# Kernel tuning notes

Measured on AMD Instinct MI355X. Metric: run time of the kernel, lower is better.

The kernel has to match this reference:

```python
import jax, jax.numpy as jnp
import numpy as np

EPS = 1e-7  # K.epsilon()
B, S, W1, W2, D = 256, 4, 64, 128, 300
HID = 4


def setup_inputs() -> dict:
    key = jax.random.key(0)
    k1, k2, k3, k4, k5, k6, k7 = jax.random.split(key, 7)
    return {
        "tuple1": jax.random.normal(k1, (B, S, W1, D), dtype=jnp.float32),
        "tuple2": jax.random.normal(k2, (B, S, W2, D), dtype=jnp.float32),
        "mask1": jax.random.randint(k3, (B, S, W1), 0, 2, dtype=jnp.int32),
        "mask2": jax.random.randint(k4, (B, S, W2), 0, 2, dtype=jnp.int32),
        "threshold": jax.random.normal(k5, (), dtype=jnp.float32),
        "W_hidden": jax.random.normal(k6, (S, HID), dtype=jnp.float32) * 0.5,
        "W_score": jax.random.normal(k7, (HID, 1), dtype=jnp.float32) * 0.5,
    }


def reference(tuple1, tuple2, mask1, mask2, threshold, W_hidden, W_score):
    # Pairwise dot-product similarity between every tuple1 word and tuple2 word per slot.
    sim = jnp.einsum("bswd,bsvd->bswv", tuple1, tuple2)  # (B, S, W1, W2)
    m1 = mask1.astype(jnp.float32)
    m2 = mask2.astype(jnp.float32)
    overlap = (sim >= threshold).astype(jnp.float32)
    overlap = overlap * m1[:, :, :, None] * m2[:, :, None, :]
    slot_overlap = jnp.sum(overlap, axis=(2, 3))  # (B, S)
    count1 = jnp.sum(m1, axis=2)  # (B, S)
    divisor = jnp.where(count1 == 0, EPS, count1)
    normalized = slot_overlap / divisor  # (B, S)
    h = jnp.tanh(normalized @ W_hidden)  # (B, HID)
    return jax.nn.sigmoid(h @ W_score)  # (B, 1)
```

## Files before the change

kernel.cpp:

```cpp
#include <hip/hip_runtime.h>
#include <math.h>

#define B_   256
#define S_   4
#define W1_  64
#define W2_  128
#define D_   300
#define HID_ 4

typedef float          fx4   __attribute__((ext_vector_type(4)));
typedef short          s16x8 __attribute__((ext_vector_type(8)));
typedef unsigned int   ux4   __attribute__((ext_vector_type(4)));

__device__ __forceinline__ unsigned bf16_rne(float x) {
    unsigned u = __float_as_uint(x);
    return (u + 0x7FFFu + ((u >> 16) & 1u)) >> 16;
}

__device__ __forceinline__ void cvt8(const fx4 x0, const fx4 x1, s16x8& hi, s16x8& lo) {
    ux4 hu, lu;
#pragma unroll
    for (int p = 0; p < 4; ++p) {
        float a = (p < 2) ? x0[2 * p]     : x1[2 * p - 4];
        float b = (p < 2) ? x0[2 * p + 1] : x1[2 * p - 3];
        unsigned ha = bf16_rne(a), hb = bf16_rne(b);
        float haf = __uint_as_float(ha << 16);
        float hbf = __uint_as_float(hb << 16);
        unsigned la = bf16_rne(a - haf), lb = bf16_rne(b - hbf);
        hu[p] = ha | (hb << 16);
        lu[p] = la | (lb << 16);
    }
    hi = __builtin_bit_cast(s16x8, hu);
    lo = __builtin_bit_cast(s16x8, lu);
}

template <int OFF>
__device__ __forceinline__ void gload(fx4& d, const float* p) {
    asm volatile("global_load_dwordx4 %0, %1, off offset:%c2"
                 : "=v"(d) : "v"(p), "i"(OFF));
}

#define FENCE  __builtin_amdgcn_sched_barrier(0)
#define WAIT24 do { asm volatile("s_waitcnt vmcnt(24)" ::: "memory"); FENCE; } while (0)
#define WAIT12 do { asm volatile("s_waitcnt vmcnt(12)" ::: "memory"); FENCE; } while (0)
#define WAIT0  do { asm volatile("s_waitcnt vmcnt(0)"  ::: "memory"); FENCE; } while (0)

#define ISSUE(T, AA, BB) do { \
    gload<(T)*128>(AA[0][0], aP0); gload<(T)*128+16>(AA[0][1], aP0); \
    gload<(T)*128>(AA[1][0], aP1); gload<(T)*128+16>(AA[1][1], aP1); \
    gload<(T)*128>(BB[0][0], bP0); gload<(T)*128+16>(BB[0][1], bP0); \
    gload<(T)*128>(BB[1][0], bP1); gload<(T)*128+16>(BB[1][1], bP1); \
    gload<(T)*128>(BB[2][0], bP2); gload<(T)*128+16>(BB[2][1], bP2); \
    gload<(T)*128>(BB[3][0], bP3); gload<(T)*128+16>(BB[3][1], bP3); \
    FENCE; } while (0)

__global__ __launch_bounds__(256, 2) void sim_count_mfma(
    const float* __restrict__ t1, const float* __restrict__ t2,
    const int* __restrict__ m1, const int* __restrict__ m2,
    const float* __restrict__ thr_p, int* __restrict__ cnt)
{
    const int slot = blockIdx.x;
    const int tid  = threadIdx.x;
    const int l    = tid & 63;
    const int w    = tid >> 6;
    const int rowHalf = w >> 1, colHalf = w & 1;
    const int lr   = l & 15;
    const int lg8  = (l >> 4) * 8;

    const float* t1b = t1 + (size_t)slot * W1_ * D_;
    const float* t2b = t2 + (size_t)slot * W2_ * D_;
    const float* aP0 = t1b + (size_t)(rowHalf * 32 +  0 + lr) * D_ + lg8;
    const float* aP1 = t1b + (size_t)(rowHalf * 32 + 16 + lr) * D_ + lg8;
    const float* bP0 = t2b + (size_t)(colHalf * 64 +  0 + lr) * D_ + lg8;
    const float* bP1 = t2b + (size_t)(colHalf * 64 + 16 + lr) * D_ + lg8;
    const float* bP2 = t2b + (size_t)(colHalf * 64 + 32 + lr) * D_ + lg8;
    const float* bP3 = t2b + (size_t)(colHalf * 64 + 48 + lr) * D_ + lg8;

    fx4 acc[2][4];
#pragma unroll
    for (int rt = 0; rt < 2; ++rt)
#pragma unroll
        for (int ct = 0; ct < 4; ++ct) {
            fx4 z; z[0] = 0.f; z[1] = 0.f; z[2] = 0.f; z[3] = 0.f;
            acc[rt][ct] = z;
        }

    auto compute = [&](fx4 (&SA)[2][2], fx4 (&SB)[4][2]) {
        s16x8 ah[2], al[2];
#pragma unroll
        for (int rt = 0; rt < 2; ++rt) cvt8(SA[rt][0], SA[rt][1], ah[rt], al[rt]);
#pragma unroll
        for (int ct = 0; ct < 4; ++ct) {
            s16x8 bh, bl;
            cvt8(SB[ct][0], SB[ct][1], bh, bl);
#pragma unroll
            for (int rt = 0; rt < 2; ++rt) {
                acc[rt][ct] = __builtin_amdgcn_mfma_f32_16x16x32_bf16(ah[rt], bh, acc[rt][ct], 0, 0, 0);
                acc[rt][ct] = __builtin_amdgcn_mfma_f32_16x16x32_bf16(ah[rt], bl, acc[rt][ct], 0, 0, 0);
                acc[rt][ct] = __builtin_amdgcn_mfma_f32_16x16x32_bf16(al[rt], bh, acc[rt][ct], 0, 0, 0);
            }
        }
    };

    fx4 A0[2][2], B0[4][2], A1[2][2], B1[4][2], A2[2][2], B2[4][2];

    ISSUE(0, A0, B0);
    ISSUE(1, A1, B1);
    ISSUE(2, A2, B2);
    WAIT24; compute(A0, B0); FENCE; ISSUE(3, A0, B0);
    WAIT24; compute(A1, B1); FENCE; ISSUE(4, A1, B1);
    WAIT24; compute(A2, B2); FENCE; ISSUE(5, A2, B2);
    WAIT24; compute(A0, B0); FENCE; ISSUE(6, A0, B0);
    WAIT24; compute(A1, B1); FENCE; ISSUE(7, A1, B1);
    WAIT24; compute(A2, B2); FENCE; ISSUE(8, A2, B2);
    WAIT24; compute(A0, B0); FENCE;
    WAIT12; compute(A1, B1); FENCE;
    WAIT0;  compute(A2, B2); FENCE;

    {
        fx4 z; z[0] = 0.f; z[1] = 0.f; z[2] = 0.f; z[3] = 0.f;
        A0[0][0] = z; A0[0][1] = z; A0[1][0] = z; A0[1][1] = z;
        B0[0][0] = z; B0[0][1] = z; B0[1][0] = z; B0[1][1] = z;
        B0[2][0] = z; B0[2][1] = z; B0[3][0] = z; B0[3][1] = z;
        if (lg8 < 16) {
            A0[0][0] = *(const fx4*)(aP0 + 288);
            A0[1][0] = *(const fx4*)(aP1 + 288);
            B0[0][0] = *(const fx4*)(bP0 + 288);
            B0[1][0] = *(const fx4*)(bP1 + 288);
            B0[2][0] = *(const fx4*)(bP2 + 288);
            B0[3][0] = *(const fx4*)(bP3 + 288);
        }
        if (lg8 == 0) {
            A0[0][1] = *(const fx4*)(aP0 + 292);
            A0[1][1] = *(const fx4*)(aP1 + 292);
            B0[0][1] = *(const fx4*)(bP0 + 292);
            B0[1][1] = *(const fx4*)(bP1 + 292);
            B0[2][1] = *(const fx4*)(bP2 + 292);
            B0[3][1] = *(const fx4*)(bP3 + 292);
        }
        compute(A0, B0);
    }

    const float thr = *thr_p;
    int am[2][4];
#pragma unroll
    for (int rt = 0; rt < 2; ++rt)
#pragma unroll
        for (int r = 0; r < 4; ++r)
            am[rt][r] = m1[slot * W1_ + rowHalf * 32 + rt * 16 + (l >> 4) * 4 + r];
    int bm[4];
#pragma unroll
    for (int ct = 0; ct < 4; ++ct)
        bm[ct] = m2[slot * W2_ + colHalf * 64 + ct * 16 + lr];

    int lc = 0;
#pragma unroll
    for (int rt = 0; rt < 2; ++rt)
#pragma unroll
        for (int ct = 0; ct < 4; ++ct)
#pragma unroll
            for (int r = 0; r < 4; ++r)
                lc += ((acc[rt][ct][r] >= thr) & (am[rt][r] != 0) & (bm[ct] != 0)) ? 1 : 0;
#pragma unroll
    for (int o = 32; o > 0; o >>= 1) lc += __shfl_down(lc, o);
    if (l == 0) atomicAdd(&cnt[slot], lc);
}

__global__ __launch_bounds__(256) void finalize_head(
    const int* __restrict__ cnt, const int* __restrict__ m1,
    const float* __restrict__ Wh,
    const float* __restrict__ Ws,
    float* __restrict__ out)
{
    int b = blockIdx.x * blockDim.x + threadIdx.x;
    if (b >= B_) return;
    float n[4];
#pragma unroll
    for (int s = 0; s < 4; ++s) {
        const int slot = b * 4 + s;
        int nA = 0;
        const int4* mp = (const int4*)(m1 + slot * W1_);
#pragma unroll
        for (int g = 0; g < 16; ++g) {
            int4 v = mp[g];
            nA += (v.x != 0) + (v.y != 0) + (v.z != 0) + (v.w != 0);
        }
        const float divisor = (nA == 0) ? 1e-7f : (float)nA;
        n[s] = (float)cnt[slot] / divisor;
    }
    float score = 0.f;
#pragma unroll
    for (int j = 0; j < HID_; ++j) {
        float h = n[0] * Wh[0 * HID_ + j] + n[1] * Wh[1 * HID_ + j]
                + n[2] * Wh[2 * HID_ + j] + n[3] * Wh[3 * HID_ + j];
        h = tanhf(h);
        score += h * Ws[j];
    }
    out[b] = 1.f / (1.f + expf(-score));
}

extern "C" void kernel_launch(void* const* d_in, const int* in_sizes, int n_in,
                              void* d_out, int out_size, void* d_ws, size_t ws_size,
                              hipStream_t stream)
{
    const float* t1  = (const float*)d_in[0];
    const float* t2  = (const float*)d_in[1];
    const int*   m1  = (const int*)d_in[2];
    const int*   m2  = (const int*)d_in[3];
    const float* thr = (const float*)d_in[4];
    const float* Wh  = (const float*)d_in[5];
    const float* Ws  = (const float*)d_in[6];
    float* out = (float*)d_out;
    int*   cnt = (int*)d_ws;

    hipMemsetAsync(cnt, 0, B_ * S_ * sizeof(int), stream);
    sim_count_mfma<<<B_ * S_, 256, 0, stream>>>(t1, t2, m1, m2, thr, cnt);
    finalize_head<<<1, 256, 0, stream>>>(cnt, m1, Wh, Ws, out);
}
```

Before: 306.9 us.

## Split each slot across eight blocks with one MFMA tile per wave

Each slot's 64x128 similarity matrix is now split over 8 blocks, and each wave computes a single 16x16 tile with a 4-deep load pipeline. Occupancy is raised to 4 blocks per CU. The goal is more parallelism and latency hiding on a latency-bound kernel. The tail K-chunk is folded into the prefetch pipeline using in-bounds loads and lane masking. The trade-off is more redundant global/L2 loads of A and B rows and more atomics.

```diff
diff --git a/kernel.cpp b/kernel.cpp
--- a/kernel.cpp
+++ b/kernel.cpp
@@ -41,129 +41,90 @@
 }
 
 #define FENCE  __builtin_amdgcn_sched_barrier(0)
-#define WAIT24 do { asm volatile("s_waitcnt vmcnt(24)" ::: "memory"); FENCE; } while (0)
-#define WAIT12 do { asm volatile("s_waitcnt vmcnt(12)" ::: "memory"); FENCE; } while (0)
-#define WAIT0  do { asm volatile("s_waitcnt vmcnt(0)"  ::: "memory"); FENCE; } while (0)
+#define WAITN(N) do { asm volatile("s_waitcnt vmcnt(" #N ")" ::: "memory"); FENCE; } while (0)
 
-#define ISSUE(T, AA, BB) do { \
-    gload<(T)*128>(AA[0][0], aP0); gload<(T)*128+16>(AA[0][1], aP0); \
-    gload<(T)*128>(AA[1][0], aP1); gload<(T)*128+16>(AA[1][1], aP1); \
-    gload<(T)*128>(BB[0][0], bP0); gload<(T)*128+16>(BB[0][1], bP0); \
-    gload<(T)*128>(BB[1][0], bP1); gload<(T)*128+16>(BB[1][1], bP1); \
-    gload<(T)*128>(BB[2][0], bP2); gload<(T)*128+16>(BB[2][1], bP2); \
-    gload<(T)*128>(BB[3][0], bP3); gload<(T)*128+16>(BB[3][1], bP3); \
-    FENCE; } while (0)
-
-__global__ __launch_bounds__(256, 2) void sim_count_mfma(
+__global__ __launch_bounds__(256, 4) void sim_count_mfma(
     const float* __restrict__ t1, const float* __restrict__ t2,
     const int* __restrict__ m1, const int* __restrict__ m2,
     const float* __restrict__ thr_p, int* __restrict__ cnt)
 {
-    const int slot = blockIdx.x;
+    const int slot = blockIdx.x >> 3;
+    const int p8   = blockIdx.x & 7;
     const int tid  = threadIdx.x;
     const int l    = tid & 63;
     const int w    = tid >> 6;
-    const int rowHalf = w >> 1, colHalf = w & 1;
+    const int rt   = (p8 >> 2) * 2 + (w >> 1);
+    const int ct   = (p8 & 3) * 2 + (w & 1);
     const int lr   = l & 15;
     const int lg8  = (l >> 4) * 8;
 
-    const float* t1b = t1 + (size_t)slot * W1_ * D_;
-    const float* t2b = t2 + (size_t)slot * W2_ * D_;
-    const float* aP0 = t1b + (size_t)(rowHalf * 32 +  0 + lr) * D_ + lg8;
-    const float* aP1 = t1b + (size_t)(rowHalf * 32 + 16 + lr) * D_ + lg8;
-    const float* bP0 = t2b + (size_t)(colHalf * 64 +  0 + lr) * D_ + lg8;
-    const float* bP1 = t2b + (size_t)(colHalf * 64 + 16 + lr) * D_ + lg8;
-    const float* bP2 = t2b + (size_t)(colHalf * 64 + 32 + lr) * D_ + lg8;
-    const float* bP3 = t2b + (size_t)(colHalf * 64 + 48 + lr) * D_ + lg8;
+    const float* aP = t1 + (size_t)slot * W1_ * D_ + (size_t)(rt * 16 + lr) * D_ + lg8;
+    const float* bP = t2 + (size_t)slot * W2_ * D_ + (size_t)(ct * 16 + lr) * D_ + lg8;
 
-    fx4 acc[2][4];
-#pragma unroll
-    for (int rt = 0; rt < 2; ++rt)
-#pragma unroll
-        for (int ct = 0; ct < 4; ++ct) {
-            fx4 z; z[0] = 0.f; z[1] = 0.f; z[2] = 0.f; z[3] = 0.f;
-            acc[rt][ct] = z;
-        }
+    fx4 acc; acc[0] = 0.f; acc[1] = 0.f; acc[2] = 0.f; acc[3] = 0.f;
 
-    auto compute = [&](fx4 (&SA)[2][2], fx4 (&SB)[4][2]) {
-        s16x8 ah[2], al[2];
-#pragma unroll
-        for (int rt = 0; rt < 2; ++rt) cvt8(SA[rt][0], SA[rt][1], ah[rt], al[rt]);
-#pragma unroll
-        for (int ct = 0; ct < 4; ++ct) {
-            s16x8 bh, bl;
-            cvt8(SB[ct][0], SB[ct][1], bh, bl);
-#pragma unroll
-            for (int rt = 0; rt < 2; ++rt) {
-                acc[rt][ct] = __builtin_amdgcn_mfma_f32_16x16x32_bf16(ah[rt], bh, acc[rt][ct], 0, 0, 0);
-                acc[rt][ct] = __builtin_amdgcn_mfma_f32_16x16x32_bf16(ah[rt], bl, acc[rt][ct], 0, 0, 0);
-                acc[rt][ct] = __builtin_amdgcn_mfma_f32_16x16x32_bf16(al[rt], bh, acc[rt][ct], 0, 0, 0);
-            }
-        }
+    fx4 S0a0, S0a1, S0b0, S0b1, S1a0, S1a1, S1b0, S1b1,
+        S2a0, S2a1, S2b0, S2b1, S3a0, S3a1, S3b0, S3b1;
+
+#define ISSUE(T, S) do { \
+    gload<(T)*128>(S##a0, aP); gload<(T)*128+16>(S##a1, aP); \
+    gload<(T)*128>(S##b0, bP); gload<(T)*128+16>(S##b1, bP); FENCE; } while (0)
+
+    auto compute = [&](fx4& a0, fx4& a1, fx4& b0, fx4& b1) {
+        s16x8 ah, al, bh, bl;
+        cvt8(a0, a1, ah, al);
+        cvt8(b0, b1, bh, bl);
+        acc = __builtin_amdgcn_mfma_f32_16x16x32_bf16(ah, bh, acc, 0, 0, 0);
+        acc = __builtin_amdgcn_mfma_f32_16x16x32_bf16(ah, bl, acc, 0, 0, 0);
+        acc = __builtin_amdgcn_mfma_f32_16x16x32_bf16(al, bh, acc, 0, 0, 0);
     };
 
-    fx4 A0[2][2], B0[4][2], A1[2][2], B1[4][2], A2[2][2], B2[4][2];
+    ISSUE(0, S0); ISSUE(1, S1); ISSUE(2, S2); ISSUE(3, S3);
 
-    ISSUE(0, A0, B0);
-    ISSUE(1, A1, B1);
-    ISSUE(2, A2, B2);
-    WAIT24; compute(A0, B0); FENCE; ISSUE(3, A0, B0);
-    WAIT24; compute(A1, B1); FENCE; ISSUE(4, A1, B1);
-    WAIT24; compute(A2, B2); FENCE; ISSUE(5, A2, B2);
-    WAIT24; compute(A0, B0); FENCE; ISSUE(6, A0, B0);
-    WAIT24; compute(A1, B1); FENCE; ISSUE(7, A1, B1);
-    WAIT24; compute(A2, B2); FENCE; ISSUE(8, A2, B2);
-    WAIT24; compute(A0, B0); FENCE;
-    WAIT12; compute(A1, B1); FENCE;
-    WAIT0;  compute(A2, B2); FENCE;
-
+    WAITN(12); compute(S0a0, S0a1, S0b0, S0b1); FENCE; ISSUE(4, S0);
+    WAITN(12); compute(S1a0, S1a1, S1b0, S1b1); FENCE; ISSUE(5, S1);
+    WAITN(12); compute(S2a0, S2a1, S2b0, S2b1); FENCE; ISSUE(6, S2);
+    WAITN(12); compute(S3a0, S3a1, S3b0, S3b1); FENCE; ISSUE(7, S3);
+    WAITN(12); compute(S0a0, S0a1, S0b0, S0b1); FENCE; ISSUE(8, S0);
+    WAITN(12); compute(S1a0, S1a1, S1b0, S1b1); FENCE;
     {
-        fx4 z; z[0] = 0.f; z[1] = 0.f; z[2] = 0.f; z[3] = 0.f;
-        A0[0][0] = z; A0[0][1] = z; A0[1][0] = z; A0[1][1] = z;
-        B0[0][0] = z; B0[0][1] = z; B0[1][0] = z; B0[1][1] = z;
-        B0[2][0] = z; B0[2][1] = z; B0[3][0] = z; B0[3][1] = z;
-        if (lg8 < 16) {
-            A0[0][0] = *(const fx4*)(aP0 + 288);
-            A0[1][0] = *(const fx4*)(aP1 + 288);
-            B0[0][0] = *(const fx4*)(bP0 + 288);
-            B0[1][0] = *(const fx4*)(bP1 + 288);
-            B0[2][0] = *(const fx4*)(bP2 + 288);
-            B0[3][0] = *(const fx4*)(bP3 + 288);
+        const float* aRow = aP - lg8;
+        const float* bRow = bP - lg8;
+        const int o1 = (lg8 == 8) ? 296 : 288;
+        const int o2 = (lg8 == 0) ? 292 : 288;
+        gload<0>(S1a0, aRow + o1);
+        gload<0>(S1a1, aRow + o2);
+        gload<0>(S1b0, bRow + o1);
+        gload<0>(S1b1, bRow + o2);
+        FENCE;
+    }
+    WAITN(12); compute(S2a0, S2a1, S2b0, S2b1); FENCE;
+    WAITN(8);  compute(S3a0, S3a1, S3b0, S3b1); FENCE;
+    WAITN(4);  compute(S0a0, S0a1, S0b0, S0b1); FENCE;
+    WAITN(0);
+    {
+        const bool k1 = (lg8 <= 8);
+        const bool k2 = (lg8 == 0);
+#pragma unroll
+        for (int e = 0; e < 4; ++e) {
+            S1a0[e] = k1 ? S1a0[e] : 0.f;  S1a1[e] = k2 ? S1a1[e] : 0.f;
+            S1b0[e] = k1 ? S1b0[e] : 0.f;  S1b1[e] = k2 ? S1b1[e] : 0.f;
         }
-        if (lg8 == 0) {
-            A0[0][1] = *(const fx4*)(aP0 + 292);
-            A0[1][1] = *(const fx4*)(aP1 + 292);
-            B0[0][1] = *(const fx4*)(bP0 + 292);
-            B0[1][1] = *(const fx4*)(bP1 + 292);
-            B0[2][1] = *(const fx4*)(bP2 + 292);
-            B0[3][1] = *(const fx4*)(bP3 + 292);
-        }
-        compute(A0, B0);
+        compute(S1a0, S1a1, S1b0, S1b1);
     }
 
     const float thr = *thr_p;
-    int am[2][4];
-#pragma unroll
-    for (int rt = 0; rt < 2; ++rt)
-#pragma unroll
-        for (int r = 0; r < 4; ++r)
-            am[rt][r] = m1[slot * W1_ + rowHalf * 32 + rt * 16 + (l >> 4) * 4 + r];
-    int bm[4];
-#pragma unroll
-    for (int ct = 0; ct < 4; ++ct)
-        bm[ct] = m2[slot * W2_ + colHalf * 64 + ct * 16 + lr];
-
+    const int bm = m2[slot * W2_ + ct * 16 + lr];
     int lc = 0;
 #pragma unroll
-    for (int rt = 0; rt < 2; ++rt)
-#pragma unroll
-        for (int ct = 0; ct < 4; ++ct)
-#pragma unroll
-            for (int r = 0; r < 4; ++r)
-                lc += ((acc[rt][ct][r] >= thr) & (am[rt][r] != 0) & (bm[ct] != 0)) ? 1 : 0;
+    for (int r = 0; r < 4; ++r) {
+        const int am = m1[slot * W1_ + rt * 16 + (l >> 4) * 4 + r];
+        lc += ((acc[r] >= thr) & (am != 0) & (bm != 0)) ? 1 : 0;
+    }
 #pragma unroll
     for (int o = 32; o > 0; o >>= 1) lc += __shfl_down(lc, o);
     if (l == 0) atomicAdd(&cnt[slot], lc);
+#undef ISSUE
 }
 
 __global__ __launch_bounds__(256) void finalize_head(
@@ -214,6 +175,6 @@
     int*   cnt = (int*)d_ws;
 
     hipMemsetAsync(cnt, 0, B_ * S_ * sizeof(int), stream);
-    sim_count_mfma<<<B_ * S_, 256, 0, stream>>>(t1, t2, m1, m2, thr, cnt);
+    sim_count_mfma<<<B_ * S_ * 8, 256, 0, stream>>>(t1, t2, m1, m2, thr, cnt);
     finalize_head<<<1, 256, 0, stream>>>(cnt, m1, Wh, Ws, out);
 }
```

Result: slower. 567.5 us (+84.9%).
